# Performance work log

Measured on AMD Instinct MI355X. Metric: run time of the kernel, lower is better.

Reference implementation:

```python
import jax, jax.numpy as jnp
import numpy as np

B, T, C, H = 4, 2048, 1024, 16
D = C // H
THETA = 10000.0
SCALE_BASE = 512.0


def _rot_tables():
    # xpos rotary tables (lucidrains rotary_embedding_torch conventions)
    inv_freq = 1.0 / (THETA ** (np.arange(0, D, 2, dtype=np.float32) / D))  # [D/2]
    seq = np.arange(T, dtype=np.float32)
    freqs = seq[:, None] * inv_freq[None, :]            # [T, D/2]
    freqs = np.repeat(freqs, 2, axis=-1)                # [T, D] interleaved pairs
    base = (np.arange(0, D, 2, dtype=np.float32) + 0.4 * D) / (1.4 * D)  # [D/2]
    power = (seq - T // 2) / SCALE_BASE                 # [T]
    scale = base[None, :] ** power[:, None]             # [T, D/2]
    scale = np.repeat(scale, 2, axis=-1)                # [T, D]
    return (jnp.asarray(np.cos(freqs)), jnp.asarray(np.sin(freqs)),
            jnp.asarray(scale))


def _rotate_half(x):
    # interleaved pair rotation: (x0, x1) -> (-x1, x0)
    x1 = x[..., 0::2]
    x2 = x[..., 1::2]
    return jnp.stack((-x2, x1), axis=-1).reshape(x.shape)


def setup_inputs() -> dict:
    key = jax.random.key(0)
    ks = jax.random.split(key, 6)
    x = jax.random.normal(ks[0], (B, T, C), dtype=jnp.float32)
    attn_mask = jax.random.randint(ks[1], (B, 1, T, T), 0, 2, dtype=jnp.int32)
    s = 1.0 / np.sqrt(C)
    Wq = jax.random.normal(ks[2], (C, C), dtype=jnp.float32) * s
    Wk = jax.random.normal(ks[3], (C, C), dtype=jnp.float32) * s
    Wv = jax.random.normal(ks[4], (C, C), dtype=jnp.float32) * s
    Wo = jax.random.normal(ks[5], (C, C), dtype=jnp.float32) * s
    return {"x": x, "attn_mask": attn_mask, "Wq": Wq, "Wk": Wk, "Wv": Wv, "Wo": Wo}


def reference(x, attn_mask, Wq, Wk, Wv, Wo):
    b, t, c = x.shape
    cos, sin, scale = _rot_tables()  # each [T, D]

    def heads(w):
        # torch Linear: y = x @ W.T ; split heads -> [b, h, t, d]
        return jnp.einsum('btc,dc->btd', x, w).reshape(b, t, H, D).transpose(0, 2, 1, 3)

    q, k, v = heads(Wq), heads(Wk), heads(Wv)
    # xpos rotary: q scaled by `scale`, k by `scale**-1`
    q = (q * cos + _rotate_half(q) * sin) * scale
    k = (k * cos + _rotate_half(k) * sin) / scale

    scores = jnp.einsum('bhqd,bhkd->bhqk', q, k) / jnp.sqrt(jnp.float32(c))
    scores = jnp.where(attn_mask == 0, jnp.float32(-10000.0), scores)
    probs = jax.nn.softmax(scores, axis=-1)  # dropout_p=0 in eval
    out = jnp.einsum('bhqk,bhkd->bhqd', probs, v)
    out = out.transpose(0, 2, 1, 3).reshape(b, t, c)
    return jnp.einsum('btc,dc->btd', out, Wo)
```

## Files before the change

### kernel.cpp

```cpp
#include <hip/hip_runtime.h>
#include <stdint.h>

#define B_ 4
#define T_ 2048
#define C_ 1024
#define H_ 16
#define D_ 64
#define M_ (B_*T_)

typedef float f4 __attribute__((ext_vector_type(4)));
typedef float f32x4 __attribute__((ext_vector_type(4)));
typedef __bf16 bf16x8 __attribute__((ext_vector_type(8)));
typedef __bf16 bf16x4 __attribute__((ext_vector_type(4)));
typedef unsigned short u16x4 __attribute__((ext_vector_type(4)));

__device__ __forceinline__ unsigned short f2bf(float f) {
  unsigned u = __builtin_bit_cast(unsigned, f);
  u += 0x7fffu + ((u >> 16) & 1u);
  return (unsigned short)(u >> 16);
}

__device__ __forceinline__ f4 mfma16(bf16x8 a, bf16x8 b, f4 c) {
  return __builtin_amdgcn_mfma_f32_16x16x32_bf16(a, b, c, 0, 0, 0);
}

__device__ __forceinline__ void gload16(const void* g, void* l) {
  __builtin_amdgcn_global_load_lds(
      (const __attribute__((address_space(1))) unsigned int*)g,
      (__attribute__((address_space(3))) unsigned int*)l, 16, 0, 0);
}

__global__ void prep_tables(float* __restrict__ cosT, float* __restrict__ sinT,
                            float* __restrict__ scT, float* __restrict__ iscT) {
  int idx = blockIdx.x * blockDim.x + threadIdx.x;
  if (idx >= T_ * (D_ / 2)) return;
  int t = idx >> 5;
  int i = idx & 31;
  float d2 = 2.0f * (float)i;
  float inv_freq = powf(10000.0f, -(d2 / 64.0f));
  float fr = (float)t * inv_freq;
  float c = cosf(fr), s = sinf(fr);
  float base = (d2 + 0.4f * 64.0f) / (1.4f * 64.0f);
  float pw = ((float)t - 1024.0f) / 512.0f;
  float sc = powf(base, pw);
  int o = t * 64 + i * 2;
  cosT[o] = c; cosT[o + 1] = c;
  sinT[o] = s; sinT[o + 1] = s;
  scT[o] = sc; scT[o + 1] = sc;
  iscT[o] = 1.0f / sc; iscT[o + 1] = 1.0f / sc;
}

__global__ void cvt_bf16(const float* __restrict__ src,
                         unsigned short* __restrict__ dst, int n4) {
  int i = blockIdx.x * blockDim.x + threadIdx.x;
  if (i >= n4) return;
  f32x4 v = *(const f32x4*)(src + (size_t)i * 4);
  u16x4 o;
  o[0] = f2bf(v[0]); o[1] = f2bf(v[1]); o[2] = f2bf(v[2]); o[3] = f2bf(v[3]);
  *(u16x4*)(dst + (size_t)i * 4) = o;
}

__global__ void pack_mask(const int* __restrict__ mask,
                          unsigned long long* __restrict__ bits) {
  int wv = (blockIdx.x * blockDim.x + threadIdx.x) >> 6;
  int lane = threadIdx.x & 63;
  size_t base = (size_t)wv * 4;
#pragma unroll
  for (int j = 0; j < 4; ++j) {
    int v = mask[(base + j) * 64 + lane];
    unsigned long long w = __ballot(v != 0);
    if (lane == 0) bits[base + j] = w;
  }
}

__global__ __launch_bounds__(256, 2)
void gemm_qkv(const unsigned short* __restrict__ A,
              const unsigned short* __restrict__ Wq,
              const unsigned short* __restrict__ Wk,
              const unsigned short* __restrict__ Wv,
              unsigned short* __restrict__ Qo,
              unsigned short* __restrict__ Ko,
              unsigned short* __restrict__ Vo,
              const float* __restrict__ cosT,
              const float* __restrict__ sinT,
              const float* __restrict__ scT,
              const float* __restrict__ iscT) {
  __shared__ __align__(16) unsigned short As[2][128 * 32];
  __shared__ __align__(16) unsigned short Bs[2][128 * 32];

  const int z = blockIdx.z;
  const unsigned short* W = (z == 0) ? Wq : (z == 1) ? Wk : Wv;

  const int tid = threadIdx.x;
  const int lane = tid & 63;
  const int wave = tid >> 6;
  const int m0 = blockIdx.y * 128;
  const int n0 = blockIdx.x * 128;
  const int wm = (wave >> 1) * 64;
  const int wn = (wave & 1) * 64;
  const int fr = lane & 15;
  const int fg = lane >> 4;

  f4 acc[4][4];
#pragma unroll
  for (int mi = 0; mi < 4; ++mi)
#pragma unroll
    for (int ni = 0; ni < 4; ++ni) acc[mi][ni] = (f4){0.f, 0.f, 0.f, 0.f};

  const int c0 = wave * 2, c1 = wave * 2 + 1;
  const int srow = lane >> 2;
  const int sslot = (lane & 3) ^ (srow & 3);
  const unsigned short* a0 = A + (size_t)(m0 + c0 * 16 + srow) * 1024 + sslot * 8;
  const unsigned short* a1 = A + (size_t)(m0 + c1 * 16 + srow) * 1024 + sslot * 8;
  const unsigned short* b0 = W + (size_t)(n0 + c0 * 16 + srow) * 1024 + sslot * 8;
  const unsigned short* b1 = W + (size_t)(n0 + c1 * 16 + srow) * 1024 + sslot * 8;

  gload16(a0, &As[0][c0 * 512]);
  gload16(a1, &As[0][c1 * 512]);
  gload16(b0, &Bs[0][c0 * 512]);
  gload16(b1, &Bs[0][c1 * 512]);
  asm volatile("s_waitcnt vmcnt(0)" ::: "memory");
  __builtin_amdgcn_s_barrier();

  for (int k0 = 0; k0 < 1024; k0 += 32) {
    const int cur = (k0 >> 5) & 1;
    if (k0 + 32 < 1024) {
      const int nxt = cur ^ 1;
      gload16(a0 + k0 + 32, &As[nxt][c0 * 512]);
      gload16(a1 + k0 + 32, &As[nxt][c1 * 512]);
      gload16(b0 + k0 + 32, &Bs[nxt][c0 * 512]);
      gload16(b1 + k0 + 32, &Bs[nxt][c1 * 512]);
    }
    bf16x8 af[4], bfr[4];
#pragma unroll
    for (int mi = 0; mi < 4; ++mi) {
      int row = wm + mi * 16 + fr;
      af[mi] = *(const bf16x8*)&As[cur][row * 32 + ((fg ^ (fr & 3)) * 8)];
    }
#pragma unroll
    for (int ni = 0; ni < 4; ++ni) {
      int row = wn + ni * 16 + fr;
      bfr[ni] = *(const bf16x8*)&Bs[cur][row * 32 + ((fg ^ (fr & 3)) * 8)];
    }
#pragma unroll
    for (int mi = 0; mi < 4; ++mi)
#pragma unroll
      for (int ni = 0; ni < 4; ++ni)
        acc[mi][ni] = mfma16(af[mi], bfr[ni], acc[mi][ni]);
    asm volatile("s_waitcnt vmcnt(0)" ::: "memory");
    __builtin_amdgcn_s_barrier();
  }

  const int frow = fg * 4;

  if (z == 2) {
#pragma unroll
    for (int mi = 0; mi < 4; ++mi) {
      int r0 = m0 + wm + mi * 16 + frow;
      int b = r0 >> 11, t0v = r0 & 2047;
#pragma unroll
      for (int ni = 0; ni < 4; ++ni) {
        int n = n0 + wn + ni * 16 + fr;
        size_t base = ((size_t)(b * 16 + (n >> 6)) * 64 + (n & 63)) * 2048 + t0v;
        u16x4 pk;
        pk[0] = f2bf(acc[mi][ni][0]);
        pk[1] = f2bf(acc[mi][ni][1]);
        pk[2] = f2bf(acc[mi][ni][2]);
        pk[3] = f2bf(acc[mi][ni][3]);
        *(u16x4*)&Vo[base] = pk;
      }
    }
  } else {
    unsigned short* O = (z == 0) ? Qo : Ko;
    const float* sT = (z == 0) ? scT : iscT;
    const float post = (z == 0) ? 0.04508443895f : 1.0f;
#pragma unroll
    for (int mi = 0; mi < 4; ++mi)
#pragma unroll
      for (int ni = 0; ni < 4; ++ni) {
        int n = n0 + wn + ni * 16 + fr;
        int d = n & 63, hh = n >> 6;
#pragma unroll
        for (int i = 0; i < 4; ++i) {
          int r = m0 + wm + mi * 16 + frow + i;
          int t = r & 2047, b = r >> 11;
          float v = acc[mi][ni][i];
          float p = __shfl_xor(v, 1);
          int o = t * 64 + d;
          float cv = cosT[o], sv = sinT[o], scv = sT[o];
          float rot = (d & 1) ? p : -p;
          float res = (v * cv + rot * sv) * scv * post;
          O[((size_t)(b * 16 + hh) * 2048 + t) * 64 + d] = f2bf(res);
        }
      }
  }
}

__global__ __launch_bounds__(256, 2)
void gemm_out(const unsigned short* __restrict__ A,
              const unsigned short* __restrict__ W,
              float* __restrict__ O) {
  __shared__ __align__(16) unsigned short As[2][128 * 32];
  __shared__ __align__(16) unsigned short Bs[2][128 * 32];

  const int tid = threadIdx.x;
  const int lane = tid & 63;
  const int wave = tid >> 6;
  const int m0 = blockIdx.y * 128;
  const int n0 = blockIdx.x * 128;
  const int wm = (wave >> 1) * 64;
  const int wn = (wave & 1) * 64;
  const int fr = lane & 15;
  const int fg = lane >> 4;

  f4 acc[4][4];
#pragma unroll
  for (int mi = 0; mi < 4; ++mi)
#pragma unroll
    for (int ni = 0; ni < 4; ++ni) acc[mi][ni] = (f4){0.f, 0.f, 0.f, 0.f};

  const int c0 = wave * 2, c1 = wave * 2 + 1;
  const int srow = lane >> 2;
  const int sslot = (lane & 3) ^ (srow & 3);
  const unsigned short* a0 = A + (size_t)(m0 + c0 * 16 + srow) * 1024 + sslot * 8;
  const unsigned short* a1 = A + (size_t)(m0 + c1 * 16 + srow) * 1024 + sslot * 8;
  const unsigned short* b0 = W + (size_t)(n0 + c0 * 16 + srow) * 1024 + sslot * 8;
  const unsigned short* b1 = W + (size_t)(n0 + c1 * 16 + srow) * 1024 + sslot * 8;

  gload16(a0, &As[0][c0 * 512]);
  gload16(a1, &As[0][c1 * 512]);
  gload16(b0, &Bs[0][c0 * 512]);
  gload16(b1, &Bs[0][c1 * 512]);
  asm volatile("s_waitcnt vmcnt(0)" ::: "memory");
  __builtin_amdgcn_s_barrier();

  for (int k0 = 0; k0 < 1024; k0 += 32) {
    const int cur = (k0 >> 5) & 1;
    if (k0 + 32 < 1024) {
      const int nxt = cur ^ 1;
      gload16(a0 + k0 + 32, &As[nxt][c0 * 512]);
      gload16(a1 + k0 + 32, &As[nxt][c1 * 512]);
      gload16(b0 + k0 + 32, &Bs[nxt][c0 * 512]);
      gload16(b1 + k0 + 32, &Bs[nxt][c1 * 512]);
    }
    bf16x8 af[4], bfr[4];
#pragma unroll
    for (int mi = 0; mi < 4; ++mi) {
      int row = wm + mi * 16 + fr;
      af[mi] = *(const bf16x8*)&As[cur][row * 32 + ((fg ^ (fr & 3)) * 8)];
    }
#pragma unroll
    for (int ni = 0; ni < 4; ++ni) {
      int row = wn + ni * 16 + fr;
      bfr[ni] = *(const bf16x8*)&Bs[cur][row * 32 + ((fg ^ (fr & 3)) * 8)];
    }
#pragma unroll
    for (int mi = 0; mi < 4; ++mi)
#pragma unroll
      for (int ni = 0; ni < 4; ++ni)
        acc[mi][ni] = mfma16(af[mi], bfr[ni], acc[mi][ni]);
    asm volatile("s_waitcnt vmcnt(0)" ::: "memory");
    __builtin_amdgcn_s_barrier();
  }

  const int frow = fg * 4;
#pragma unroll
  for (int mi = 0; mi < 4; ++mi)
#pragma unroll
    for (int ni = 0; ni < 4; ++ni) {
      int n = n0 + wn + ni * 16 + fr;
#pragma unroll
      for (int i = 0; i < 4; ++i) {
        int r = m0 + wm + mi * 16 + frow + i;
        O[(size_t)r * 1024 + n] = acc[mi][ni][i];
      }
    }
}

__global__ __launch_bounds__(512, 6)
void attn_fwd(const unsigned short* __restrict__ Q,
              const unsigned short* __restrict__ K,
              const unsigned short* __restrict__ Vt,
              const unsigned long long* __restrict__ Mbits,
              unsigned short* __restrict__ Oa) {
  __shared__ __align__(16) unsigned short Ks[2][64 * 64];
  __shared__ __align__(16) unsigned short Vs[2][64 * 64];
  __shared__ __align__(16) unsigned short Ps[8][16][72];

  const int bid0 = blockIdx.x;
  const int wg = (bid0 & 7) * 128 + (bid0 >> 3);
  const int qt = wg & 15;
  const int h = (wg >> 4) & 15;
  const int b = wg >> 8;
  const int tid = threadIdx.x;
  const int lane = tid & 63;
  const int wave = tid >> 6;
  const int fr = lane & 15;
  const int fg = lane >> 4;
  const int frow = fg * 4;

  const unsigned short* Qb = Q + (size_t)(b * 16 + h) * (2048 * 64);
  const unsigned short* Kb = K + (size_t)(b * 16 + h) * (2048 * 64);
  const unsigned short* Vb = Vt + (size_t)(b * 16 + h) * (64 * 2048);

  const int q0 = qt * 128 + wave * 16;

  bf16x8 qf0 = *(const bf16x8*)&Qb[(q0 + fr) * 64 + fg * 8];
  bf16x8 qf1 = *(const bf16x8*)&Qb[(q0 + fr) * 64 + 32 + fg * 8];

  f4 po[4];
#pragma unroll
  for (int nd = 0; nd < 4; ++nd) po[nd] = (f4){0.f, 0.f, 0.f, 0.f};
  float lr = 0.f;

  const int krow0 = lane >> 3;
  const int kslot = (lane & 7) ^ (krow0 & 7);
  const unsigned short* kg = Kb + (size_t)(wave * 8 + krow0) * 64 + kslot * 8;
  const unsigned short* vg = Vb + (size_t)(wave * 8 + krow0) * 2048 + kslot * 8;

  const unsigned long long* mrow = Mbits + (size_t)(b * 2048 + q0 + fr) * 32;

  gload16(kg, &Ks[0][wave * 512]);
  gload16(vg, &Vs[0][wave * 512]);
  asm volatile("s_waitcnt vmcnt(0)" ::: "memory");
  __builtin_amdgcn_s_barrier();

  for (int kt = 0; kt < 32; ++kt) {
    const int cur = kt & 1;

    unsigned long long w = mrow[kt];

    if (kt < 31) {
      const int nxt = cur ^ 1;
      gload16(kg + (size_t)(kt + 1) * 4096, &Ks[nxt][wave * 512]);
      gload16(vg + (kt + 1) * 64, &Vs[nxt][wave * 512]);
    }

    f4 sf[4];
    __builtin_amdgcn_s_setprio(1);
#pragma unroll
    for (int nf = 0; nf < 4; ++nf) {
      int krow = nf * 16 + fr;
      int sw = krow & 7;
      bf16x8 kf0 = *(const bf16x8*)&Ks[cur][krow * 64 + ((fg ^ sw) * 8)];
      bf16x8 kf1 = *(const bf16x8*)&Ks[cur][krow * 64 + (((4 + fg) ^ sw) * 8)];
      f4 a = (f4){0.f, 0.f, 0.f, 0.f};
      a = mfma16(kf0, qf0, a);
      a = mfma16(kf1, qf1, a);
      sf[nf] = a;
    }
    __builtin_amdgcn_s_setprio(0);

    unsigned lo = (unsigned)w >> (fg * 4);
    unsigned hi = (unsigned)(w >> 32) >> (fg * 4);
#pragma unroll
    for (int nf = 0; nf < 4; ++nf) {
      unsigned wsel = (nf & 2) ? hi : lo;
#pragma unroll
      for (int i = 0; i < 4; ++i) {
        float p = exp2f(sf[nf][i]);
        if (!((wsel >> (((nf & 1) << 4) + i)) & 1)) p = 0.f;
        sf[nf][i] = p;
        lr += p;
      }
    }

#pragma unroll
    for (int nf = 0; nf < 4; ++nf) {
      bf16x4 pk = { (__bf16)sf[nf][0], (__bf16)sf[nf][1],
                    (__bf16)sf[nf][2], (__bf16)sf[nf][3] };
      *(bf16x4*)&Ps[wave][fr][nf * 16 + frow] = pk;
    }
    bf16x8 pf0 = *(const bf16x8*)&Ps[wave][fr][fg * 8];
    bf16x8 pf1 = *(const bf16x8*)&Ps[wave][fr][32 + fg * 8];

    __builtin_amdgcn_s_setprio(1);
#pragma unroll
    for (int nd = 0; nd < 4; ++nd) {
      int vrow = nd * 16 + fr;
      int sw = vrow & 7;
      bf16x8 vf0 = *(const bf16x8*)&Vs[cur][vrow * 64 + ((fg ^ sw) * 8)];
      bf16x8 vf1 = *(const bf16x8*)&Vs[cur][vrow * 64 + (((4 + fg) ^ sw) * 8)];
      po[nd] = mfma16(pf0, vf0, po[nd]);
      po[nd] = mfma16(pf1, vf1, po[nd]);
    }
    __builtin_amdgcn_s_setprio(0);

    asm volatile("s_waitcnt vmcnt(0)" ::: "memory");
    __builtin_amdgcn_s_barrier();
  }

  lr += __shfl_xor(lr, 16);
  lr += __shfl_xor(lr, 32);
  float lv[4];
#pragma unroll
  for (int i = 0; i < 4; ++i) lv[i] = __shfl(lr, frow + i);
#pragma unroll
  for (int nd = 0; nd < 4; ++nd) {
    int col = h * 64 + nd * 16 + fr;
#pragma unroll
    for (int i = 0; i < 4; ++i) {
      int r = b * 2048 + q0 + frow + i;
      float o = po[nd][i] / lv[i];
      Oa[(size_t)r * 1024 + col] = f2bf(o);
    }
  }
}

extern "C" void kernel_launch(void* const* d_in, const int* in_sizes, int n_in,
                              void* d_out, int out_size, void* d_ws, size_t ws_size,
                              hipStream_t stream) {
  const float* x = (const float*)d_in[0];
  const int* mask = (const int*)d_in[1];
  const float* Wq = (const float*)d_in[2];
  const float* Wk = (const float*)d_in[3];
  const float* Wv = (const float*)d_in[4];
  const float* Wo = (const float*)d_in[5];
  float* out = (float*)d_out;
  char* ws = (char*)d_ws;

  float* cosT = (float*)(ws + 0x0);
  float* sinT = (float*)(ws + 0x80000);
  float* scT  = (float*)(ws + 0x100000);
  float* iscT = (float*)(ws + 0x180000);
  unsigned long long* mbits = (unsigned long long*)(ws + 0x0);
  unsigned short* xb  = (unsigned short*)(ws + 0x200000);
  unsigned short* wqb = (unsigned short*)(ws + 0x1200000);
  unsigned short* wkb = (unsigned short*)(ws + 0x1400000);
  unsigned short* wvb = (unsigned short*)(ws + 0x1600000);
  unsigned short* wob = (unsigned short*)(ws + 0x1800000);
  unsigned short* Qb  = (unsigned short*)(ws + 0x1A00000);
  unsigned short* Kb  = (unsigned short*)(ws + 0x2A00000);
  unsigned short* Vtb = (unsigned short*)(ws + 0x3A00000);
  unsigned short* Aob = (unsigned short*)(ws + 0x4A00000);

  prep_tables<<<(T_ * (D_ / 2) + 255) / 256, 256, 0, stream>>>(cosT, sinT, scT, iscT);
  cvt_bf16<<<(M_ * C_ / 4 + 255) / 256, 256, 0, stream>>>(x, xb, M_ * C_ / 4);
  cvt_bf16<<<(C_ * C_ / 4 + 255) / 256, 256, 0, stream>>>(Wq, wqb, C_ * C_ / 4);
  cvt_bf16<<<(C_ * C_ / 4 + 255) / 256, 256, 0, stream>>>(Wk, wkb, C_ * C_ / 4);
  cvt_bf16<<<(C_ * C_ / 4 + 255) / 256, 256, 0, stream>>>(Wv, wvb, C_ * C_ / 4);
  cvt_bf16<<<(C_ * C_ / 4 + 255) / 256, 256, 0, stream>>>(Wo, wob, C_ * C_ / 4);

  dim3 gq(C_ / 128, M_ / 128, 3);
  gemm_qkv<<<gq, 256, 0, stream>>>(xb, wqb, wkb, wvb, Qb, Kb, Vtb,
                                   cosT, sinT, scT, iscT);

  pack_mask<<<16384, 256, 0, stream>>>(mask, mbits);

  attn_fwd<<<B_ * H_ * (T_ / 128), 512, 0, stream>>>(Qb, Kb, Vtb, mbits, Aob);

  dim3 go(C_ / 128, M_ / 128);
  gemm_out<<<go, 256, 0, stream>>>(Aob, wob, out);
}
```

Measured before the change: 410.8 us.

## Fuse conversions, remap GEMM blocks per XCD, compute softmax sums via MFMA

Replaces the five bf16 conversion launches with one combined kernel to cut launch overhead. Both GEMMs get an XCD-aware block-index remap for better L2 locality, a higher launch-bounds occupancy target and a 2x unrolled k-loop. The attention kernel computes row sums with an MFMA against a ones vector instead of scalar adds and shuffles, uses raw exp2 and rcp intrinsics, and unrolls its main loop. This risks register pressure under the tighter occupancy bound and slightly lower precision, since the row sums now use bf16-rounded probabilities.

```diff
diff --git a/kernel.cpp b/kernel.cpp
--- a/kernel.cpp
+++ b/kernel.cpp
@@ -50,10 +50,23 @@
   iscT[o] = 1.0f / sc; iscT[o + 1] = 1.0f / sc;
 }
 
-__global__ void cvt_bf16(const float* __restrict__ src,
-                         unsigned short* __restrict__ dst, int n4) {
-  int i = blockIdx.x * blockDim.x + threadIdx.x;
-  if (i >= n4) return;
+__global__ void cvt_all(const float* __restrict__ x,
+                        const float* __restrict__ wq, const float* __restrict__ wk,
+                        const float* __restrict__ wv, const float* __restrict__ wo,
+                        unsigned short* __restrict__ xb,
+                        unsigned short* __restrict__ wqb, unsigned short* __restrict__ wkb,
+                        unsigned short* __restrict__ wvb, unsigned short* __restrict__ wob) {
+  int bid = blockIdx.x;
+  const float* src; unsigned short* dst; int i;
+  if (bid < 8192) {
+    src = x; dst = xb; i = bid * 256 + threadIdx.x;
+  } else {
+    int r = bid - 8192;
+    int w = r >> 10;
+    src = (w == 0) ? wq : (w == 1) ? wk : (w == 2) ? wv : wo;
+    dst = (w == 0) ? wqb : (w == 1) ? wkb : (w == 2) ? wvb : wob;
+    i = (r & 1023) * 256 + threadIdx.x;
+  }
   f32x4 v = *(const f32x4*)(src + (size_t)i * 4);
   u16x4 o;
   o[0] = f2bf(v[0]); o[1] = f2bf(v[1]); o[2] = f2bf(v[2]); o[3] = f2bf(v[3]);
@@ -73,7 +86,7 @@
   }
 }
 
-__global__ __launch_bounds__(256, 2)
+__global__ __launch_bounds__(256, 3)
 void gemm_qkv(const unsigned short* __restrict__ A,
               const unsigned short* __restrict__ Wq,
               const unsigned short* __restrict__ Wk,
@@ -88,14 +101,20 @@
   __shared__ __align__(16) unsigned short As[2][128 * 32];
   __shared__ __align__(16) unsigned short Bs[2][128 * 32];
 
-  const int z = blockIdx.z;
+  const int id = blockIdx.x + 8 * blockIdx.y + 512 * blockIdx.z;
+  const int xcd = id & 7;
+  const int rest = id >> 3;
+  const int by = xcd * 8 + (rest & 7);
+  const int bx = (rest >> 3) & 7;
+  const int z = rest >> 6;
+
   const unsigned short* W = (z == 0) ? Wq : (z == 1) ? Wk : Wv;
 
   const int tid = threadIdx.x;
   const int lane = tid & 63;
   const int wave = tid >> 6;
-  const int m0 = blockIdx.y * 128;
-  const int n0 = blockIdx.x * 128;
+  const int m0 = by * 128;
+  const int n0 = bx * 128;
   const int wm = (wave >> 1) * 64;
   const int wn = (wave & 1) * 64;
   const int fr = lane & 15;
@@ -122,6 +141,7 @@
   asm volatile("s_waitcnt vmcnt(0)" ::: "memory");
   __builtin_amdgcn_s_barrier();
 
+#pragma unroll 2
   for (int k0 = 0; k0 < 1024; k0 += 32) {
     const int cur = (k0 >> 5) & 1;
     if (k0 + 32 < 1024) {
@@ -196,18 +216,24 @@
   }
 }
 
-__global__ __launch_bounds__(256, 2)
+__global__ __launch_bounds__(256, 3)
 void gemm_out(const unsigned short* __restrict__ A,
               const unsigned short* __restrict__ W,
               float* __restrict__ O) {
   __shared__ __align__(16) unsigned short As[2][128 * 32];
   __shared__ __align__(16) unsigned short Bs[2][128 * 32];
 
+  const int id = blockIdx.x + 8 * blockIdx.y;
+  const int xcd = id & 7;
+  const int rest = id >> 3;
+  const int by = xcd * 8 + (rest & 7);
+  const int bx = (rest >> 3) & 7;
+
   const int tid = threadIdx.x;
   const int lane = tid & 63;
   const int wave = tid >> 6;
-  const int m0 = blockIdx.y * 128;
-  const int n0 = blockIdx.x * 128;
+  const int m0 = by * 128;
+  const int n0 = bx * 128;
   const int wm = (wave >> 1) * 64;
   const int wn = (wave & 1) * 64;
   const int fr = lane & 15;
@@ -234,6 +260,7 @@
   asm volatile("s_waitcnt vmcnt(0)" ::: "memory");
   __builtin_amdgcn_s_barrier();
 
+#pragma unroll 2
   for (int k0 = 0; k0 < 1024; k0 += 32) {
     const int cur = (k0 >> 5) & 1;
     if (k0 + 32 < 1024) {
@@ -308,10 +335,14 @@
   bf16x8 qf0 = *(const bf16x8*)&Qb[(q0 + fr) * 64 + fg * 8];
   bf16x8 qf1 = *(const bf16x8*)&Qb[(q0 + fr) * 64 + 32 + fg * 8];
 
+  bf16x8 onesf;
+#pragma unroll
+  for (int j = 0; j < 8; ++j) onesf[j] = (__bf16)1.0f;
+
   f4 po[4];
 #pragma unroll
   for (int nd = 0; nd < 4; ++nd) po[nd] = (f4){0.f, 0.f, 0.f, 0.f};
-  float lr = 0.f;
+  f4 lsum = (f4){0.f, 0.f, 0.f, 0.f};
 
   const int krow0 = lane >> 3;
   const int kslot = (lane & 7) ^ (krow0 & 7);
@@ -325,6 +356,7 @@
   asm volatile("s_waitcnt vmcnt(0)" ::: "memory");
   __builtin_amdgcn_s_barrier();
 
+#pragma unroll 2
   for (int kt = 0; kt < 32; ++kt) {
     const int cur = kt & 1;
 
@@ -356,25 +388,24 @@
 #pragma unroll
     for (int nf = 0; nf < 4; ++nf) {
       unsigned wsel = (nf & 2) ? hi : lo;
-#pragma unroll
-      for (int i = 0; i < 4; ++i) {
-        float p = exp2f(sf[nf][i]);
-        if (!((wsel >> (((nf & 1) << 4) + i)) & 1)) p = 0.f;
-        sf[nf][i] = p;
-        lr += p;
-      }
-    }
-
-#pragma unroll
-    for (int nf = 0; nf < 4; ++nf) {
-      bf16x4 pk = { (__bf16)sf[nf][0], (__bf16)sf[nf][1],
-                    (__bf16)sf[nf][2], (__bf16)sf[nf][3] };
+      float p0 = __builtin_amdgcn_exp2f(sf[nf][0]);
+      float p1 = __builtin_amdgcn_exp2f(sf[nf][1]);
+      float p2 = __builtin_amdgcn_exp2f(sf[nf][2]);
+      float p3 = __builtin_amdgcn_exp2f(sf[nf][3]);
+      const int sh = (nf & 1) << 4;
+      if (!((wsel >> (sh + 0)) & 1)) p0 = 0.f;
+      if (!((wsel >> (sh + 1)) & 1)) p1 = 0.f;
+      if (!((wsel >> (sh + 2)) & 1)) p2 = 0.f;
+      if (!((wsel >> (sh + 3)) & 1)) p3 = 0.f;
+      bf16x4 pk = { (__bf16)p0, (__bf16)p1, (__bf16)p2, (__bf16)p3 };
       *(bf16x4*)&Ps[wave][fr][nf * 16 + frow] = pk;
     }
     bf16x8 pf0 = *(const bf16x8*)&Ps[wave][fr][fg * 8];
     bf16x8 pf1 = *(const bf16x8*)&Ps[wave][fr][32 + fg * 8];
 
     __builtin_amdgcn_s_setprio(1);
+    lsum = mfma16(pf0, onesf, lsum);
+    lsum = mfma16(pf1, onesf, lsum);
 #pragma unroll
     for (int nd = 0; nd < 4; ++nd) {
       int vrow = nd * 16 + fr;
@@ -390,18 +421,16 @@
     __builtin_amdgcn_s_barrier();
   }
 
-  lr += __shfl_xor(lr, 16);
-  lr += __shfl_xor(lr, 32);
-  float lv[4];
-#pragma unroll
-  for (int i = 0; i < 4; ++i) lv[i] = __shfl(lr, frow + i);
+  float inv[4];
+#pragma unroll
+  for (int i = 0; i < 4; ++i) inv[i] = __builtin_amdgcn_rcpf(lsum[i]);
 #pragma unroll
   for (int nd = 0; nd < 4; ++nd) {
     int col = h * 64 + nd * 16 + fr;
 #pragma unroll
     for (int i = 0; i < 4; ++i) {
       int r = b * 2048 + q0 + frow + i;
-      float o = po[nd][i] / lv[i];
+      float o = po[nd][i] * inv[i];
       Oa[(size_t)r * 1024 + col] = f2bf(o);
     }
   }
@@ -435,11 +464,8 @@
   unsigned short* Aob = (unsigned short*)(ws + 0x4A00000);
 
   prep_tables<<<(T_ * (D_ / 2) + 255) / 256, 256, 0, stream>>>(cosT, sinT, scT, iscT);
-  cvt_bf16<<<(M_ * C_ / 4 + 255) / 256, 256, 0, stream>>>(x, xb, M_ * C_ / 4);
-  cvt_bf16<<<(C_ * C_ / 4 + 255) / 256, 256, 0, stream>>>(Wq, wqb, C_ * C_ / 4);
-  cvt_bf16<<<(C_ * C_ / 4 + 255) / 256, 256, 0, stream>>>(Wk, wkb, C_ * C_ / 4);
-  cvt_bf16<<<(C_ * C_ / 4 + 255) / 256, 256, 0, stream>>>(Wv, wvb, C_ * C_ / 4);
-  cvt_bf16<<<(C_ * C_ / 4 + 255) / 256, 256, 0, stream>>>(Wo, wob, C_ * C_ / 4);
+  cvt_all<<<8192 + 4096, 256, 0, stream>>>(x, Wq, Wk, Wv, Wo,
+                                           xb, wqb, wkb, wvb, wob);
 
   dim3 gq(C_ / 128, M_ / 128, 3);
   gemm_qkv<<<gq, 256, 0, stream>>>(xb, wqb, wkb, wvb, Qb, Kb, Vtb,
```

Result: faster. 364.7 us (-11.2%).
